# Optimization experiments

Hardware: AMD Instinct MI355X
Metric: run time of the kernel (lower is better)

Reference implementation:

```python
import jax, jax.numpy as jnp
import numpy as np

ALPHA = 3.0
EPS = 1e-6
LOSS_WEIGHT = 1.0
N = 1_000_000


def _cross(a, b):
    return a[..., 0] * b[..., 1] - a[..., 1] * b[..., 0]


def _corners(b):
    # b: (n,5) -> (n,4,2) corners in CCW-ish order
    x, y, w, h, a = (b[:, i] for i in range(5))
    c, s = jnp.cos(a), jnp.sin(a)
    dx = jnp.stack([-w, w, w, -w], -1) * 0.5  # (n,4)
    dy = jnp.stack([-h, -h, h, h], -1) * 0.5
    X = x[:, None] + dx * c[:, None] - dy * s[:, None]
    Y = y[:, None] + dx * s[:, None] + dy * c[:, None]
    return jnp.stack([X, Y], -1)


def _inside(pts, box):
    # pts: (n,4,2) world coords; box: (n,5). Test via box-local frame.
    x, y, w, h, a = (box[:, i] for i in range(5))
    c, s = jnp.cos(a), jnp.sin(a)
    rel = pts - jnp.stack([x, y], -1)[:, None]
    lx = rel[..., 0] * c[:, None] + rel[..., 1] * s[:, None]
    ly = -rel[..., 0] * s[:, None] + rel[..., 1] * c[:, None]
    m = 1e-5  # numeric margin
    return (jnp.abs(lx) <= w[:, None] * 0.5 + m) & (jnp.abs(ly) <= h[:, None] * 0.5 + m)


def _rot_inter_area(b1, b2):
    c1, c2 = _corners(b1), _corners(b2)            # (n,4,2)
    r = jnp.roll(c1, -1, axis=1) - c1               # edge vectors box1
    s = jnp.roll(c2, -1, axis=1) - c2               # edge vectors box2
    p = c1[:, :, None]                              # (n,4,1,2)
    q = c2[:, None]                                 # (n,1,4,2)
    rr = r[:, :, None]
    ss = s[:, None]
    den = _cross(rr, ss)                            # (n,4,4)
    den_safe = jnp.where(jnp.abs(den) < 1e-12, 1.0, den)
    qp = q - p
    t = _cross(qp, ss) / den_safe
    u = _cross(qp, rr) / den_safe
    ok = (jnp.abs(den) > 1e-12) & (t >= 0.0) & (t <= 1.0) & (u >= 0.0) & (u <= 1.0)
    ipts = p + t[..., None] * rr                    # (n,4,4,2) edge-edge intersections

    n = b1.shape[0]
    pts = jnp.concatenate([ipts.reshape(n, 16, 2), c1, c2], axis=1)          # (n,24,2)
    mask = jnp.concatenate([ok.reshape(n, 16), _inside(c1, b2), _inside(c2, b1)], axis=1)
    maskf = mask.astype(pts.dtype)
    cnt = maskf.sum(1)                              # (n,)
    center = (pts * maskf[..., None]).sum(1) / jnp.maximum(cnt, 1.0)[:, None]

    ang = jnp.arctan2(pts[..., 1] - center[:, None, 1], pts[..., 0] - center[:, None, 0])
    ang = jnp.where(mask, ang, 1e9)                 # invalid points sort last
    order = jnp.argsort(ang, axis=1)
    pts_s = jnp.take_along_axis(pts, order[..., None], axis=1)
    mask_s = jnp.take_along_axis(mask, order, axis=1)
    first = pts_s[:, 0:1]
    pts_s = jnp.where(mask_s[..., None], pts_s, first)  # collapse invalid -> zero shoelace terms
    nxt = jnp.roll(pts_s, -1, axis=1)
    area = 0.5 * jnp.abs(_cross(pts_s, nxt).sum(1))
    return jnp.where(cnt >= 3.0, area, 0.0)


def setup_inputs() -> dict:
    key = jax.random.key(0)
    k1, k2, k3, k4, k5, k6 = jax.random.split(key, 6)
    xy = jax.random.uniform(k1, (N, 2), jnp.float32, 0.0, 512.0)
    wh = jax.random.uniform(k2, (N, 2), jnp.float32, 4.0, 64.0)
    ang = jax.random.uniform(k3, (N, 1), jnp.float32, -np.pi / 2, np.pi / 2)
    pred = jnp.concatenate([xy, wh, ang], axis=1)
    # target: perturbed pred so IoUs are non-trivial
    txy = xy + jax.random.normal(k4, (N, 2), jnp.float32) * 4.0
    twh = wh * jax.random.uniform(k5, (N, 2), jnp.float32, 0.8, 1.25)
    tang = ang + jax.random.normal(k6, (N, 1), jnp.float32) * 0.2
    target = jnp.concatenate([txy, twh, tang], axis=1)
    return {"pred": pred, "target": target}


def reference(pred, target):
    inter = _rot_inter_area(pred, target)
    a1 = pred[:, 2] * pred[:, 3]
    a2 = target[:, 2] * target[:, 3]
    ious = inter / (a1 + a2 - inter)
    ious = jnp.maximum(ious, EPS)                   # clamp(min=eps)
    loss = 1.0 - ious ** ALPHA                      # linear=True branch
    return LOSS_WEIGHT * loss.mean()                # reduction='mean'
```

## Files before the change

kernel.cpp:

```cpp
#include <hip/hip_runtime.h>
#include <math.h>

#define EPS_IOU 1e-6f
#define BLOCK 256
#define EPB 512

__global__ void zero_out_kernel(float* out) { out[0] = 0.0f; }

__device__ __forceinline__ float clip_len(float p0x, float p0y, float dx, float dy,
                                          float rcx, float rcy, float ux, float uy,
                                          float hw, float hh) {
  const float rx = p0x - rcx, ry = p0y - rcy;
  const float bu = rx * ux + ry * uy;
  const float bv = -rx * uy + ry * ux;
  const float au = dx * ux + dy * uy;
  const float av = -dx * uy + dy * ux;
  const float iu = __builtin_amdgcn_rcpf(au);
  const float iv = __builtin_amdgcn_rcpf(av);
  const float t0 = (-hw - bu) * iu;
  const float t1 = (hw - bu) * iu;
  const float t2 = (-hh - bv) * iv;
  const float t3 = (hh - bv) * iv;
  const float lo = fmaxf(fmaxf(fminf(t0, t1), fminf(t2, t3)), 0.0f);
  const float hi = fminf(fminf(fmaxf(t0, t1), fmaxf(t2, t3)), 1.0f);
  return fmaxf(hi - lo, 0.0f);
}

__device__ __forceinline__ float pair_loss(const float* __restrict__ b1,
                                           const float* __restrict__ b2) {
  const float x1 = b1[0], y1 = b1[1], w1 = b1[2], h1 = b1[3], t1 = b1[4];
  const float x2 = b2[0], y2 = b2[1], w2 = b2[2], h2 = b2[3], t2 = b2[4];

  float s1, c1, s2, c2;
  __sincosf(t1, &s1, &c1);
  __sincosf(t2, &s2, &c2);

  const float ox = 0.5f * (x1 + x2), oy = 0.5f * (y1 + y2);
  const float a1x = x1 - ox, a1y = y1 - oy;
  const float a2x = x2 - ox, a2y = y2 - oy;

  const float hw1 = 0.5f * w1, hh1 = 0.5f * h1;
  const float hw2 = 0.5f * w2, hh2 = 0.5f * h2;

  float Ax[4], Ay[4], Bx[4], By[4];
  {
    const float dxs1[4] = {-hw1, hw1, hw1, -hw1};
    const float dys1[4] = {-hh1, -hh1, hh1, hh1};
    const float dxs2[4] = {-hw2, hw2, hw2, -hw2};
    const float dys2[4] = {-hh2, -hh2, hh2, hh2};
#pragma unroll
    for (int k = 0; k < 4; ++k) {
      Ax[k] = a1x + dxs1[k] * c1 - dys1[k] * s1;
      Ay[k] = a1y + dxs1[k] * s1 + dys1[k] * c1;
      Bx[k] = a2x + dxs2[k] * c2 - dys2[k] * s2;
      By[k] = a2y + dxs2[k] * s2 + dys2[k] * c2;
    }
  }

  float acc = 0.0f;
#pragma unroll
  for (int k = 0; k < 4; ++k) {
    const int kn = (k + 1) & 3;
    {
      const float dx = Ax[kn] - Ax[k], dy = Ay[kn] - Ay[k];
      const float len = clip_len(Ax[k], Ay[k], dx, dy, a2x, a2y, c2, s2, hw2, hh2);
      acc += (Ax[k] * dy - Ay[k] * dx) * len;
    }
    {
      const float dx = Bx[kn] - Bx[k], dy = By[kn] - By[k];
      const float len = clip_len(Bx[k], By[k], dx, dy, a1x, a1y, c1, s1, hw1, hh1);
      acc += (Bx[k] * dy - By[k] * dx) * len;
    }
  }
  const float inter = fmaxf(0.5f * acc, 0.0f);

  const float uni = w1 * h1 + w2 * h2 - inter;
  float iou = inter * __builtin_amdgcn_rcpf(uni);
  iou = fmaxf(iou, EPS_IOU);
  return 1.0f - iou * iou * iou;
}

__global__ __launch_bounds__(256) void rot_iou_loss_kernel(
    const float* __restrict__ pred, const float* __restrict__ target,
    float* __restrict__ out, int n, float inv_n) {
  __shared__ float lp[EPB * 5];
  __shared__ float lt[EPB * 5];

  const int tid = threadIdx.x;
  const long base5 = (long)blockIdx.x * (EPB * 5);
  const long total5 = (long)n * 5;

  const float4* p4 = (const float4*)(pred + base5);
  const float4* t4 = (const float4*)(target + base5);
#pragma unroll
  for (int it = 0; it < 3; ++it) {
    const int idx4 = it * BLOCK + tid;
    if (idx4 < EPB * 5 / 4) {
      const long g = base5 + (long)idx4 * 4;
      if (g + 3 < total5) {
        ((float4*)lp)[idx4] = p4[idx4];
        ((float4*)lt)[idx4] = t4[idx4];
      } else {
#pragma unroll
        for (int k = 0; k < 4; ++k) {
          const bool ok = (g + k) < total5;
          lp[idx4 * 4 + k] = ok ? pred[g + k] : 0.0f;
          lt[idx4 * 4 + k] = ok ? target[g + k] : 0.0f;
        }
      }
    }
  }
  __syncthreads();

  float loss = 0.0f;
#pragma unroll
  for (int e = 0; e < 2; ++e) {
    const int local = tid + e * BLOCK;
    const long gi = (long)blockIdx.x * EPB + local;
    if (gi < n) loss += pair_loss(&lp[local * 5], &lt[local * 5]);
  }

#pragma unroll
  for (int off = 32; off > 0; off >>= 1) loss += __shfl_down(loss, off, 64);

  __syncthreads();
  const int lane = tid & 63;
  const int wid = tid >> 6;
  if (lane == 0) lp[wid] = loss;
  __syncthreads();
  if (tid == 0) {
    const float bsum = lp[0] + lp[1] + lp[2] + lp[3];
    atomicAdd(out, bsum * inv_n);
  }
}

extern "C" void kernel_launch(void* const* d_in, const int* in_sizes, int n_in,
                              void* d_out, int out_size, void* d_ws, size_t ws_size,
                              hipStream_t stream) {
  const float* pred = (const float*)d_in[0];
  const float* target = (const float*)d_in[1];
  float* out = (float*)d_out;
  const int n = in_sizes[0] / 5;

  zero_out_kernel<<<1, 1, 0, stream>>>(out);
  const int grid = (n + EPB - 1) / EPB;
  rot_iou_loss_kernel<<<grid, BLOCK, 0, stream>>>(pred, target, out, n,
                                                  1.0f / (float)n);
}
```

Baseline: 102.7 us.

## Load boxes directly into registers and replace atomics with two-stage reduction

Each thread now handles four box pairs and reads their 20 contiguous floats straight into registers as five float4 loads, replacing the staging through shared memory and the block-wide barrier. The per-block atomicAdd onto one output is replaced by per-block partial sums in workspace and a single-block final reduction kernel, which also removes the zero-init launch. Per-thread float4 loads are strided by 80 bytes across lanes, so coalescing is weaker than the cooperative shared-memory load, and the grid shrinks to about 977 blocks, which lowers parallelism.

```diff
diff --git a/kernel.cpp b/kernel.cpp
--- a/kernel.cpp
+++ b/kernel.cpp
@@ -3,9 +3,8 @@
 
 #define EPS_IOU 1e-6f
 #define BLOCK 256
-#define EPB 512
-
-__global__ void zero_out_kernel(float* out) { out[0] = 0.0f; }
+#define BPT 4
+#define EPB (BLOCK * BPT)
 
 __device__ __forceinline__ float clip_len(float p0x, float p0y, float dx, float dy,
                                           float rcx, float rcy, float ux, float uy,
@@ -26,8 +25,7 @@
   return fmaxf(hi - lo, 0.0f);
 }
 
-__device__ __forceinline__ float pair_loss(const float* __restrict__ b1,
-                                           const float* __restrict__ b2) {
+__device__ __forceinline__ float pair_loss(const float* b1, const float* b2) {
   const float x1 = b1[0], y1 = b1[1], w1 = b1[2], h1 = b1[3], t1 = b1[4];
   const float x2 = b2[0], y2 = b2[1], w2 = b2[2], h2 = b2[3], t2 = b2[4];
 
@@ -82,56 +80,66 @@
 
 __global__ __launch_bounds__(256) void rot_iou_loss_kernel(
     const float* __restrict__ pred, const float* __restrict__ target,
-    float* __restrict__ out, int n, float inv_n) {
-  __shared__ float lp[EPB * 5];
-  __shared__ float lt[EPB * 5];
+    float* __restrict__ block_sums, int n) {
+  const int tid = threadIdx.x;
+  const long g0 = ((long)blockIdx.x * BLOCK + tid) * BPT;
 
-  const int tid = threadIdx.x;
-  const long base5 = (long)blockIdx.x * (EPB * 5);
-  const long total5 = (long)n * 5;
-
-  const float4* p4 = (const float4*)(pred + base5);
-  const float4* t4 = (const float4*)(target + base5);
+  float loss = 0.0f;
+  if (g0 + BPT - 1 < n) {
+    float fp[20], ft[20];
+    const float4* p4 = (const float4*)(pred + g0 * 5);
+    const float4* t4 = (const float4*)(target + g0 * 5);
 #pragma unroll
-  for (int it = 0; it < 3; ++it) {
-    const int idx4 = it * BLOCK + tid;
-    if (idx4 < EPB * 5 / 4) {
-      const long g = base5 + (long)idx4 * 4;
-      if (g + 3 < total5) {
-        ((float4*)lp)[idx4] = p4[idx4];
-        ((float4*)lt)[idx4] = t4[idx4];
-      } else {
+    for (int q = 0; q < 5; ++q) {
+      ((float4*)fp)[q] = p4[q];
+      ((float4*)ft)[q] = t4[q];
+    }
 #pragma unroll
-        for (int k = 0; k < 4; ++k) {
-          const bool ok = (g + k) < total5;
-          lp[idx4 * 4 + k] = ok ? pred[g + k] : 0.0f;
-          lt[idx4 * 4 + k] = ok ? target[g + k] : 0.0f;
+    for (int j = 0; j < BPT; ++j) loss += pair_loss(&fp[j * 5], &ft[j * 5]);
+  } else {
+#pragma unroll
+    for (int j = 0; j < BPT; ++j) {
+      const long gi = g0 + j;
+      if (gi < n) {
+        float bp[5], bt[5];
+#pragma unroll
+        for (int k = 0; k < 5; ++k) {
+          bp[k] = pred[gi * 5 + k];
+          bt[k] = target[gi * 5 + k];
         }
+        loss += pair_loss(bp, bt);
       }
     }
-  }
-  __syncthreads();
-
-  float loss = 0.0f;
-#pragma unroll
-  for (int e = 0; e < 2; ++e) {
-    const int local = tid + e * BLOCK;
-    const long gi = (long)blockIdx.x * EPB + local;
-    if (gi < n) loss += pair_loss(&lp[local * 5], &lt[local * 5]);
   }
 
 #pragma unroll
   for (int off = 32; off > 0; off >>= 1) loss += __shfl_down(loss, off, 64);
 
-  __syncthreads();
+  __shared__ float wsum[4];
   const int lane = tid & 63;
   const int wid = tid >> 6;
-  if (lane == 0) lp[wid] = loss;
+  if (lane == 0) wsum[wid] = loss;
   __syncthreads();
   if (tid == 0) {
-    const float bsum = lp[0] + lp[1] + lp[2] + lp[3];
-    atomicAdd(out, bsum * inv_n);
+    block_sums[blockIdx.x] = wsum[0] + wsum[1] + wsum[2] + wsum[3];
   }
+}
+
+__global__ __launch_bounds__(256) void final_reduce_kernel(
+    const float* __restrict__ block_sums, float* __restrict__ out, int nb,
+    float inv_n) {
+  const int tid = threadIdx.x;
+  float s = 0.0f;
+  for (int i = tid; i < nb; i += 256) s += block_sums[i];
+#pragma unroll
+  for (int off = 32; off > 0; off >>= 1) s += __shfl_down(s, off, 64);
+
+  __shared__ float wsum[4];
+  const int lane = tid & 63;
+  const int wid = tid >> 6;
+  if (lane == 0) wsum[wid] = s;
+  __syncthreads();
+  if (tid == 0) out[0] = (wsum[0] + wsum[1] + wsum[2] + wsum[3]) * inv_n;
 }
 
 extern "C" void kernel_launch(void* const* d_in, const int* in_sizes, int n_in,
@@ -140,10 +148,11 @@
   const float* pred = (const float*)d_in[0];
   const float* target = (const float*)d_in[1];
   float* out = (float*)d_out;
+  float* bsums = (float*)d_ws;
   const int n = in_sizes[0] / 5;
 
-  zero_out_kernel<<<1, 1, 0, stream>>>(out);
   const int grid = (n + EPB - 1) / EPB;
-  rot_iou_loss_kernel<<<grid, BLOCK, 0, stream>>>(pred, target, out, n,
-                                                  1.0f / (float)n);
+  rot_iou_loss_kernel<<<grid, BLOCK, 0, stream>>>(pred, target, bsums, n);
+  final_reduce_kernel<<<1, BLOCK, 0, stream>>>(bsums, out, grid,
+                                               1.0f / (float)n);
 }
```

Measured after the change: 90.00 us. 1.14x faster.
